# Kernel tuning notes

Hardware: AMD Instinct MI355X
Metric: run time of the kernel (lower is better)

The kernel has to match this reference:

```python
import jax, jax.numpy as jnp
import numpy as np
import math

B, H, L, D = 2, 16, 2048, 128
NEG = float(-2**32 + 1)  # module uses -2**32+1 instead of -inf to avoid softmax NaN on fully-masked rows


def setup_inputs() -> dict:
    key = jax.random.key(0)
    kq, kk, kv, km, kp = jax.random.split(key, 5)
    return {
        "Q": jax.random.normal(kq, (B, H, L, D), dtype=jnp.float32),
        "K": jax.random.normal(kk, (B, H, L, D), dtype=jnp.float32),
        "V": jax.random.normal(kv, (B, H, L, D), dtype=jnp.float32),
        "attn_mask": jax.random.normal(km, (L, L), dtype=jnp.float32),  # additive bias mask
        "padding_mask": jax.random.randint(kp, (B, L), 0, 2).astype(bool),  # True -> masked
    }


def reference(Q, K, V, attn_mask, padding_mask):
    scale = math.sqrt(Q.shape[-1])
    # energy: [B, H, Lq, Lk]
    energy = jnp.einsum("bhqd,bhkd->bhqk", Q, K) / scale
    energy = energy + attn_mask[None, None, :, :]
    energy = jnp.where(padding_mask[:, None, None, :], NEG, energy)
    attention_weight = jax.nn.softmax(energy, axis=-1)
    # dropout=None in eval semantics -> identity
    x = jnp.einsum("bhqk,bhkd->bhqd", attention_weight, V)
    return (x, attention_weight)
```

## Files before the change

kernel.cpp:

```cpp
#include <hip/hip_runtime.h>


typedef __attribute__((ext_vector_type(8))) __bf16 bf16x8;
typedef __attribute__((ext_vector_type(4))) float f32x4;

#define L_SEQ 2048
#define D_H   128
#define R_Q   128
#define C_K   64
#define NTHR  512
#define KPITCH 136
#define VPITCH 72
#define NKT   (L_SEQ / C_K)

__device__ __forceinline__ unsigned short f2bf(float f) {
    unsigned int u = __float_as_uint(f);
    unsigned int r = (u + 0x7FFFu + ((u >> 16) & 1u)) >> 16;
    return (unsigned short)r;
}

__device__ __forceinline__ float fexp2(float x) {
#if __has_builtin(__builtin_amdgcn_exp2f)
    return __builtin_amdgcn_exp2f(x);
#else
    return exp2f(x);
#endif
}

__device__ __forceinline__ float rsum16(float v) {
#pragma unroll
    for (int o = 1; o < 16; o <<= 1) v += __shfl_xor(v, o, 64);
    return v;
}

union BF8 {
    bf16x8 v;
    unsigned short s[8];
    uint4 u;
};

__global__ __launch_bounds__(NTHR, 4) void attn_kernel(
    const float* __restrict__ Q, const float* __restrict__ K,
    const float* __restrict__ V, const float* __restrict__ mask,
    const int* __restrict__ pad, float* __restrict__ Xout,
    float* __restrict__ Pout)
{
    __shared__ unsigned short Ks[C_K * KPITCH];
    __shared__ unsigned short Vt[D_H * VPITCH];
    __shared__ unsigned short Ps[R_Q * VPITCH];
    __shared__ float PadB[L_SEQ];

    const int tid  = threadIdx.x;
    const int wave = tid >> 6;
    const int lane = tid & 63;
    const int quad = lane >> 4;
    const int l16  = lane & 15;

    const int bh = blockIdx.x & 31;
    const int qt = blockIdx.x >> 5;
    const int b  = bh >> 4;

    const float LOG2E  = 1.44269504088896340736f;
    const float SCALE2 = 0.08838834764831845f * 1.44269504088896340736f;

    const float* Kg0 = K + (long long)bh * L_SEQ * D_H;
    const float* Vg0 = V + (long long)bh * L_SEQ * D_H;

    BF8 qf[4];
    {
        const float4* qrow = reinterpret_cast<const float4*>(
            Q + ((long long)bh * L_SEQ + qt * R_Q + wave * 16 + l16) * D_H);
#pragma unroll
        for (int kb = 0; kb < 4; ++kb) {
            float4 a = qrow[kb * 8 + quad * 2];
            float4 c = qrow[kb * 8 + quad * 2 + 1];
            qf[kb].s[0] = f2bf(a.x); qf[kb].s[1] = f2bf(a.y);
            qf[kb].s[2] = f2bf(a.z); qf[kb].s[3] = f2bf(a.w);
            qf[kb].s[4] = f2bf(c.x); qf[kb].s[5] = f2bf(c.y);
            qf[kb].s[6] = f2bf(c.z); qf[kb].s[7] = f2bf(c.w);
        }
    }
#pragma unroll
    for (int i = 0; i < 4; ++i) {
        int idx = tid + i * NTHR;
        PadB[idx] = pad[b * L_SEQ + idx] ? -INFINITY : 0.0f;
    }

    auto stageK = [&](int kt) {
        const float4* Kg = reinterpret_cast<const float4*>(Kg0 + (long long)kt * C_K * D_H);
#pragma unroll
        for (int i = 0; i < 2; ++i) {
            int c = tid + i * NTHR;
            int row = c >> 4, off = (c & 15) * 8;
            float4 a = Kg[c * 2];
            float4 d = Kg[c * 2 + 1];
            BF8 t;
            t.s[0] = f2bf(a.x); t.s[1] = f2bf(a.y); t.s[2] = f2bf(a.z); t.s[3] = f2bf(a.w);
            t.s[4] = f2bf(d.x); t.s[5] = f2bf(d.y); t.s[6] = f2bf(d.z); t.s[7] = f2bf(d.w);
            *reinterpret_cast<uint4*>(&Ks[row * KPITCH + off]) = t.u;
        }
    };
    auto stageV = [&](int kt) {
        const float* Vg = Vg0 + (long long)kt * C_K * D_H;
        int c = tid & 127;
#pragma unroll
        for (int i = 0; i < 2; ++i) {
            int key0 = (((tid >> 7) + i * 4) << 3);
            BF8 t;
#pragma unroll
            for (int j = 0; j < 8; ++j)
                t.s[j] = f2bf(Vg[(key0 + j) * D_H + c]);
            *reinterpret_cast<uint4*>(&Vt[c * VPITCH + key0]) = t.u;
        }
    };

    auto computeS = [&](f32x4* sacc) {
        f32x4 z4 = {0.f, 0.f, 0.f, 0.f};
#pragma unroll
        for (int ct = 0; ct < 4; ++ct) sacc[ct] = z4;
#pragma unroll
        for (int kb = 0; kb < 4; ++kb) {
#pragma unroll
            for (int ct = 0; ct < 4; ++ct) {
                bf16x8 bk = *reinterpret_cast<const bf16x8*>(
                    &Ks[(ct * 16 + l16) * KPITCH + kb * 32 + quad * 8]);
                sacc[ct] = __builtin_amdgcn_mfma_f32_16x16x32_bf16(qf[kb].v, bk, sacc[ct], 0, 0, 0);
            }
        }
    };

    const long long qrow0 = (long long)(qt * R_Q + wave * 16 + quad * 4);
    const float* maskBase = mask + qrow0 * L_SEQ;

    float lpart[4] = {0.f, 0.f, 0.f, 0.f};
    for (int kt = 0; kt < NKT; ++kt) {
        __syncthreads();
        stageK(kt);
        __syncthreads();
        f32x4 sacc[4];
        computeS(sacc);
        float mk[4][4], pb[4];
#pragma unroll
        for (int ct = 0; ct < 4; ++ct) {
            int kc = kt * C_K + ct * 16 + l16;
            pb[ct] = PadB[kc];
#pragma unroll
            for (int r = 0; r < 4; ++r) mk[ct][r] = maskBase[(long long)r * L_SEQ + kc];
        }
#pragma unroll
        for (int ct = 0; ct < 4; ++ct)
#pragma unroll
            for (int r = 0; r < 4; ++r) {
                float m2 = fmaf(mk[ct][r], LOG2E, pb[ct]);
                float e2 = fmaf(sacc[ct][r], SCALE2, m2);
                lpart[r] += fexp2(e2);
            }
    }

    float rinv[4];
#pragma unroll
    for (int r = 0; r < 4; ++r) {
        float l = rsum16(lpart[r]);
        rinv[r] = (l > 0.f) ? (1.0f / l) : 0.f;
    }

    f32x4 oacc[8];
    {
        f32x4 z4 = {0.f, 0.f, 0.f, 0.f};
#pragma unroll
        for (int ct = 0; ct < 8; ++ct) oacc[ct] = z4;
    }
    float* PoutBase = Pout + ((long long)bh * L_SEQ + (qt * R_Q + wave * 16 + quad * 4)) * L_SEQ;

    for (int kt = 0; kt < NKT; ++kt) {
        __syncthreads();
        stageK(kt);
        stageV(kt);
        __syncthreads();
        f32x4 sacc[4];
        computeS(sacc);
        float mk[4][4], pb[4];
#pragma unroll
        for (int ct = 0; ct < 4; ++ct) {
            int kc = kt * C_K + ct * 16 + l16;
            pb[ct] = PadB[kc];
#pragma unroll
            for (int r = 0; r < 4; ++r) mk[ct][r] = maskBase[(long long)r * L_SEQ + kc];
        }
#pragma unroll
        for (int ct = 0; ct < 4; ++ct) {
            int kc = kt * C_K + ct * 16 + l16;
#pragma unroll
            for (int r = 0; r < 4; ++r) {
                float m2 = fmaf(mk[ct][r], LOG2E, pb[ct]);
                float e2 = fmaf(sacc[ct][r], SCALE2, m2);
                float p  = fexp2(e2) * rinv[r];
                __builtin_nontemporal_store(p, &PoutBase[(long long)r * L_SEQ + kc]);
                Ps[(wave * 16 + quad * 4 + r) * VPITCH + ct * 16 + l16] = f2bf(p);
            }
        }
#pragma unroll
        for (int kd = 0; kd < 2; ++kd) {
            bf16x8 ap = *reinterpret_cast<const bf16x8*>(
                &Ps[(wave * 16 + l16) * VPITCH + kd * 32 + quad * 8]);
#pragma unroll
            for (int ct = 0; ct < 8; ++ct) {
                bf16x8 bv = *reinterpret_cast<const bf16x8*>(
                    &Vt[(ct * 16 + l16) * VPITCH + kd * 32 + quad * 8]);
                oacc[ct] = __builtin_amdgcn_mfma_f32_16x16x32_bf16(ap, bv, oacc[ct], 0, 0, 0);
            }
        }
    }

    float* Xg = Xout + ((long long)bh * L_SEQ + qt * R_Q + wave * 16 + quad * 4) * D_H;
#pragma unroll
    for (int ct = 0; ct < 8; ++ct)
#pragma unroll
        for (int r = 0; r < 4; ++r)
            __builtin_nontemporal_store(oacc[ct][r], &Xg[r * D_H + ct * 16 + l16]);
}

extern "C" void kernel_launch(void* const* d_in, const int* in_sizes, int n_in,
                              void* d_out, int out_size, void* d_ws, size_t ws_size,
                              hipStream_t stream) {
    const float* Q    = (const float*)d_in[0];
    const float* K    = (const float*)d_in[1];
    const float* V    = (const float*)d_in[2];
    const float* mask = (const float*)d_in[3];
    const int*   pad  = (const int*)d_in[4];
    float* Xout = (float*)d_out;
    float* Pout = (float*)d_out + (long long)2 * 16 * 2048 * 128;
    attn_kernel<<<dim3(512), dim3(NTHR), 0, stream>>>(Q, K, V, mask, pad, Xout, Pout);
}
```

Baseline: 907.3 us.

## Prefetch next K/V tile into registers and use lightweight barriers

Splits the K and V staging into a global-load phase and a convert-and-write-to-LDS phase. The loads for tile kt+1 are issued into registers while tile kt is being computed, hiding global memory latency. __syncthreads is replaced with a barrier that waits only on LDS counters and is fenced by sched_barrier, so the in-flight global prefetch is not drained at each sync. The mask loads are also moved ahead of the QK MFMA. This costs about 32 extra VGPRs per thread at a launch bound of 4 blocks of 512 threads, which risks spills or lower occupancy.

```diff
diff --git a/kernel.cpp b/kernel.cpp
--- a/kernel.cpp
+++ b/kernel.cpp
@@ -31,6 +31,13 @@
 #pragma unroll
     for (int o = 1; o < 16; o <<= 1) v += __shfl_xor(v, o, 64);
     return v;
+}
+
+__device__ __forceinline__ void block_sync() {
+    __builtin_amdgcn_sched_barrier(0);
+    asm volatile("s_waitcnt lgkmcnt(0)");
+    __builtin_amdgcn_s_barrier();
+    __builtin_amdgcn_sched_barrier(0);
 }
 
 union BF8 {
@@ -86,30 +93,50 @@
         PadB[idx] = pad[b * L_SEQ + idx] ? -INFINITY : 0.0f;
     }
 
-    auto stageK = [&](int kt) {
+    float4 kpre[4];
+    float  vpre[16];
+
+    auto issueK = [&](int kt) {
         const float4* Kg = reinterpret_cast<const float4*>(Kg0 + (long long)kt * C_K * D_H);
+#pragma unroll
+        for (int i = 0; i < 2; ++i) {
+            int c = tid + i * NTHR;
+            kpre[2 * i]     = Kg[c * 2];
+            kpre[2 * i + 1] = Kg[c * 2 + 1];
+        }
+    };
+    auto writeK = [&]() {
 #pragma unroll
         for (int i = 0; i < 2; ++i) {
             int c = tid + i * NTHR;
             int row = c >> 4, off = (c & 15) * 8;
-            float4 a = Kg[c * 2];
-            float4 d = Kg[c * 2 + 1];
+            float4 a = kpre[2 * i];
+            float4 d = kpre[2 * i + 1];
             BF8 t;
             t.s[0] = f2bf(a.x); t.s[1] = f2bf(a.y); t.s[2] = f2bf(a.z); t.s[3] = f2bf(a.w);
             t.s[4] = f2bf(d.x); t.s[5] = f2bf(d.y); t.s[6] = f2bf(d.z); t.s[7] = f2bf(d.w);
             *reinterpret_cast<uint4*>(&Ks[row * KPITCH + off]) = t.u;
         }
     };
-    auto stageV = [&](int kt) {
+    auto issueV = [&](int kt) {
         const float* Vg = Vg0 + (long long)kt * C_K * D_H;
         int c = tid & 127;
 #pragma unroll
         for (int i = 0; i < 2; ++i) {
             int key0 = (((tid >> 7) + i * 4) << 3);
+#pragma unroll
+            for (int j = 0; j < 8; ++j)
+                vpre[i * 8 + j] = Vg[(key0 + j) * D_H + c];
+        }
+    };
+    auto writeV = [&]() {
+        int c = tid & 127;
+#pragma unroll
+        for (int i = 0; i < 2; ++i) {
+            int key0 = (((tid >> 7) + i * 4) << 3);
             BF8 t;
 #pragma unroll
-            for (int j = 0; j < 8; ++j)
-                t.s[j] = f2bf(Vg[(key0 + j) * D_H + c]);
+            for (int j = 0; j < 8; ++j) t.s[j] = f2bf(vpre[i * 8 + j]);
             *reinterpret_cast<uint4*>(&Vt[c * VPITCH + key0]) = t.u;
         }
     };
@@ -133,12 +160,12 @@
     const float* maskBase = mask + qrow0 * L_SEQ;
 
     float lpart[4] = {0.f, 0.f, 0.f, 0.f};
+    issueK(0);
     for (int kt = 0; kt < NKT; ++kt) {
-        __syncthreads();
-        stageK(kt);
-        __syncthreads();
-        f32x4 sacc[4];
-        computeS(sacc);
+        block_sync();
+        writeK();
+        if (kt + 1 < NKT) issueK(kt + 1);
+        block_sync();
         float mk[4][4], pb[4];
 #pragma unroll
         for (int ct = 0; ct < 4; ++ct) {
@@ -147,6 +174,8 @@
 #pragma unroll
             for (int r = 0; r < 4; ++r) mk[ct][r] = maskBase[(long long)r * L_SEQ + kc];
         }
+        f32x4 sacc[4];
+        computeS(sacc);
 #pragma unroll
         for (int ct = 0; ct < 4; ++ct)
 #pragma unroll
@@ -172,13 +201,14 @@
     }
     float* PoutBase = Pout + ((long long)bh * L_SEQ + (qt * R_Q + wave * 16 + quad * 4)) * L_SEQ;
 
+    issueK(0);
+    issueV(0);
     for (int kt = 0; kt < NKT; ++kt) {
-        __syncthreads();
-        stageK(kt);
-        stageV(kt);
-        __syncthreads();
-        f32x4 sacc[4];
-        computeS(sacc);
+        block_sync();
+        writeK();
+        writeV();
+        if (kt + 1 < NKT) { issueK(kt + 1); issueV(kt + 1); }
+        block_sync();
         float mk[4][4], pb[4];
 #pragma unroll
         for (int ct = 0; ct < 4; ++ct) {
@@ -187,6 +217,8 @@
 #pragma unroll
             for (int r = 0; r < 4; ++r) mk[ct][r] = maskBase[(long long)r * L_SEQ + kc];
         }
+        f32x4 sacc[4];
+        computeS(sacc);
 #pragma unroll
         for (int ct = 0; ct < 4; ++ct) {
             int kc = kt * C_K + ct * 16 + l16;
```

Measured after the change: 1.093 ms. 1.2x slower.
